# Kernel tuning notes

Hardware: AMD Instinct MI355X
Metric: run time of the kernel (lower is better)

The kernel has to match this reference:

```python
import jax, jax.numpy as jnp
import numpy as np
import math

B, H, S, D = 2, 8, 1024, 384
LAMBDA_INIT = 0.8 - 0.6 * math.exp(-0.3 * 1)  # depth = 1


def _clin(xr, xi, wr, wi, br=None, bi=None):
    # complex linear: (xr + i xi) @ (wr + i wi)^T + (br + i bi)
    o_r = jnp.einsum('bhse,de->bhsd', xr, wr) - jnp.einsum('bhse,de->bhsd', xi, wi)
    o_i = jnp.einsum('bhse,de->bhsd', xr, wi) + jnp.einsum('bhse,de->bhsd', xi, wr)
    if br is not None:
        o_r = o_r + br
        o_i = o_i + bi
    return o_r, o_i


def _attn_w(qr, qi, kr, ki, scale):
    # complex score magnitude -> softmax
    s_r = jnp.einsum('bhqd,bhkd->bhqk', qr, kr) + jnp.einsum('bhqd,bhkd->bhqk', qi, ki)
    s_i = jnp.einsum('bhqd,bhkd->bhqk', qi, kr) - jnp.einsum('bhqd,bhkd->bhqk', qr, ki)
    return jax.nn.softmax(jnp.sqrt(s_r ** 2 + s_i ** 2 + 1e-8) * scale, axis=-1)


def setup_inputs() -> dict:
    key = jax.random.key(0)
    ks = jax.random.split(key, 32)
    n = lambda k, sh, std=1.0: jax.random.normal(k, sh, dtype=jnp.float32) * std
    sd = 1.0 / math.sqrt(D)
    inp = {
        'q_r': n(ks[0], (B, H, S, D)), 'q_i': n(ks[1], (B, H, S, D)),
        'k_r': n(ks[2], (B, H, S, D)), 'k_i': n(ks[3], (B, H, S, D)),
        'v_r': n(ks[4], (B, H, S, D)), 'v_i': n(ks[5], (B, H, S, D)),
        'pe_q_r': n(ks[6], (B, H, S, D)), 'pe_q_i': n(ks[7], (B, H, S, D)),
        'pe_k_r': n(ks[8], (B, H, S, D)), 'pe_k_i': n(ks[9], (B, H, S, D)),
        'wq_r': n(ks[10], (2 * D, D), sd), 'wq_i': n(ks[11], (2 * D, D), sd),
        'bq_r': jnp.zeros((2 * D,), jnp.float32), 'bq_i': jnp.zeros((2 * D,), jnp.float32),
        'wk_r': n(ks[12], (D, D), sd), 'wk_i': n(ks[13], (D, D), sd),
        'bk_r': jnp.zeros((D,), jnp.float32), 'bk_i': jnp.zeros((D,), jnp.float32),
        'wv_r': n(ks[14], (D, D), sd), 'wv_i': n(ks[15], (D, D), sd),
        'bv_r': jnp.zeros((D,), jnp.float32), 'bv_i': jnp.zeros((D,), jnp.float32),
        'wg_r': n(ks[16], (D, D), sd), 'wg_i': n(ks[17], (D, D), sd),
        'bg_r': jnp.zeros((D,), jnp.float32), 'bg_i': jnp.zeros((D,), jnp.float32),
        'wo_r': n(ks[18], (D, D), sd), 'wo_i': n(ks[19], (D, D), sd),
        'bo_r': jnp.zeros((D,), jnp.float32), 'bo_i': jnp.zeros((D,), jnp.float32),
        'lam_q1': n(ks[20], (D,), 0.1), 'lam_k1': n(ks[21], (D,), 0.1),
        'lam_q2': n(ks[22], (D,), 0.1), 'lam_k2': n(ks[23], (D,), 0.1),
        'subln_w': jnp.ones((2 * D,), jnp.float32),
    }
    return inp


def reference(q_r, q_i, k_r, k_i, v_r, v_i, pe_q_r, pe_q_i, pe_k_r, pe_k_i,
              wq_r, wq_i, bq_r, bq_i, wk_r, wk_i, bk_r, bk_i,
              wv_r, wv_i, bv_r, bv_i, wg_r, wg_i, bg_r, bg_i,
              wo_r, wo_i, bo_r, bo_i, lam_q1, lam_k1, lam_q2, lam_k2, subln_w):
    scale = D ** (-0.5)
    qp_r, qp_i = _clin(q_r, q_i, wq_r, wq_i, bq_r, bq_i)   # [B,H,S,2D]
    kp_r, kp_i = _clin(k_r, k_i, wk_r, wk_i, bk_r, bk_i)   # [B,H,S,D]
    vp_r, vp_i = _clin(v_r, v_i, wv_r, wv_i, bv_r, bv_i)
    qp_r = qp_r + jnp.concatenate([pe_q_r, pe_q_r], axis=-1)
    qp_i = qp_i + jnp.concatenate([pe_q_i, pe_q_i], axis=-1)
    kp_r = kp_r + pe_k_r
    kp_i = kp_i + pe_k_i
    q1_r, q2_r = jnp.split(qp_r, 2, axis=-1)
    q1_i, q2_i = jnp.split(qp_i, 2, axis=-1)
    w1 = _attn_w(q1_r, q1_i, kp_r, kp_i, scale)
    w2 = _attn_w(q2_r, q2_i, kp_r, kp_i, scale)
    a1_r = jnp.einsum('bhqk,bhkd->bhqd', w1, vp_r)
    a1_i = jnp.einsum('bhqk,bhkd->bhqd', w1, vp_i)
    a2_r = jnp.einsum('bhqk,bhkd->bhqd', w2, vp_r)
    a2_i = jnp.einsum('bhqk,bhkd->bhqd', w2, vp_i)
    cat_r = jnp.concatenate([a1_r, a2_r], axis=-1)
    cat_i = jnp.concatenate([a1_i, a2_i], axis=-1)
    # complex RMSNorm (SubLN) over 2D dim
    rms = jnp.sqrt(jnp.mean(cat_r ** 2 + cat_i ** 2, axis=-1, keepdims=True) + 1e-5)
    cat_r = cat_r / rms * subln_w
    cat_i = cat_i / rms * subln_w
    a1_r, a2_r = jnp.split(cat_r, 2, axis=-1)
    a1_i, a2_i = jnp.split(cat_i, 2, axis=-1)
    lam1 = jnp.exp(jnp.sum(lam_q1 * lam_k1))
    lam2 = jnp.exp(jnp.sum(lam_q2 * lam_k2))
    lam = jax.nn.sigmoid(lam1 - lam2 + LAMBDA_INIT)
    out_r = a1_r - lam * a2_r
    out_i = a1_i - lam * a2_i
    g_r, g_i = _clin(q_r, q_i, wg_r, wg_i, bg_r, bg_i)
    out_r, out_i = g_r * out_r - g_i * out_i, g_r * out_i + g_i * out_r
    out_r, out_i = _clin(out_r, out_i, wo_r, wo_i, bo_r, bo_i)
    return (out_r, out_i)
```

## Files before the change

kernel.cpp:

```cpp
#include <hip/hip_runtime.h>
#include <cstdint>


typedef _Float16 f16;
typedef __attribute__((ext_vector_type(8))) _Float16 f16x8;
typedef __attribute__((ext_vector_type(4))) _Float16 f16x4;
typedef __attribute__((ext_vector_type(4))) float    f32x4;

#define NROW      16384L
#define HALF_OUT  6291456L
#define SCALE_QK  0.05103103630798288f
#define LAMBDA_INIT 0.35550906759096926f

__device__ __forceinline__ void gl2lds16(const void* g, void* l) {
  __builtin_amdgcn_global_load_lds(
      (const __attribute__((address_space(1))) void*)(uintptr_t)g,
      (__attribute__((address_space(3))) void*)(uint32_t)(uintptr_t)l,
      16, 0, 0);
}

enum { MODE_PROJ = 0, MODE_VT = 1, MODE_OUT = 2, MODE_PV = 3 };

template <int MODE>
__launch_bounds__(256, 2)
__global__ void gemm128(const f16* __restrict__ A, int lda,
                        const f16* __restrict__ W, int ldw,
                        const float* __restrict__ bias,
                        const f16* __restrict__ pe16, int pelim,
                        void* __restrict__ outp, void* __restrict__ outp2,
                        int ldo, int K, int gx)
{
  __shared__ f16 As[2][128 * 64];
  __shared__ f16 Bs[2][128 * 64];
  const int t    = threadIdx.x;
  const int lane = t & 63;
  const int wave = t >> 6;
  const int bid  = blockIdx.x;
  const int xcd  = bid & 7;
  const int per  = bid >> 3;

  long row0, col0;
  const f16 *Ab, *Wb;
  int bh = 0;
  if (MODE == MODE_PV) {
    bh = xcd * 2 + per / 96;
    const int rem = per % 96;
    row0 = (long)(rem / 6) * 128;
    col0 = (long)(rem % 6) * 128;
    const int slab = bh + (row0 >= 1024 ? 16 : 0);
    Ab = A + ((long)slab << 20) + (row0 & 1023) * (long)lda;
    Wb = W + (long)bh * 768 * 1024 + col0 * (long)ldw;
  } else {
    row0 = (long)(xcd * 16 + per / gx) * 128;
    col0 = (long)(per % gx) * 128;
    Ab = A + row0 * (long)lda;
    Wb = W + col0 * (long)ldw;
  }

  const int wm = (wave >> 1) * 64;
  const int wn = (wave & 1) * 64;
  const int lm = lane & 15;
  const int l4 = lane >> 4;

  f32x4 acc[4][4] = {};

  auto stage = [&](int kk, int sub) {
#pragma unroll
    for (int p = 0; p < 4; ++p) {
      int sg = p * 256 + t;
      int r = sg >> 3, cl = sg & 7, cg = cl ^ (r & 7);
      gl2lds16(Ab + (long)r * lda + kk + cg * 8, &As[sub][sg * 8]);
      gl2lds16(Wb + (long)r * ldw + kk + cg * 8, &Bs[sub][sg * 8]);
    }
  };

  const int NT = K >> 6;
  stage(0, 0);
  stage(64, 1);
  int cur = 0;
  for (int it = 0; it < NT; ++it) {
    if (it + 1 < NT) asm volatile("s_waitcnt vmcnt(8)" ::: "memory");
    else             asm volatile("s_waitcnt vmcnt(0)" ::: "memory");
    __builtin_amdgcn_s_barrier();
#pragma unroll
    for (int ks = 0; ks < 2; ++ks) {
      f16x8 bfr[4];
#pragma unroll
      for (int nt = 0; nt < 4; ++nt) {
        int rr = wn + nt * 16 + lm;
        bfr[nt] = *(const f16x8*)&Bs[cur][rr * 64 + (((ks * 4 + l4) ^ (rr & 7)) << 3)];
      }
#pragma unroll
      for (int mt = 0; mt < 4; ++mt) {
        int rr = wm + mt * 16 + lm;
        f16x8 afr = *(const f16x8*)&As[cur][rr * 64 + (((ks * 4 + l4) ^ (rr & 7)) << 3)];
#pragma unroll
        for (int nt = 0; nt < 4; ++nt)
          acc[mt][nt] = __builtin_amdgcn_mfma_f32_16x16x32_f16(afr, bfr[nt], acc[mt][nt], 0, 0, 0);
      }
    }
    __builtin_amdgcn_s_barrier();
    if (it + 2 < NT) stage((it + 2) << 6, cur);
    cur ^= 1;
  }

  const int lm4 = l4 * 4;
  const int ln  = lm;
#pragma unroll
  for (int mt = 0; mt < 4; ++mt) {
#pragma unroll
    for (int nt = 0; nt < 4; ++nt) {
      int col = (int)col0 + wn + nt * 16 + ln;
      if (MODE == MODE_VT) {
        long rowb = row0 + wm + mt * 16 + lm4;
        long vbh = rowb >> 10, sx = rowb & 1023;
        f16x4 v;
#pragma unroll
        for (int r = 0; r < 4; ++r) v[r] = (f16)(acc[mt][nt][r] + bias[col]);
        *(f16x4*)&((f16*)outp)[(vbh * 768 + col) * 1024 + sx] = v;
      } else if (MODE == MODE_PV) {
#pragma unroll
        for (int r = 0; r < 4; ++r) {
          long grow = row0 + wm + mt * 16 + lm4 + r;
          f16 val = (f16)acc[mt][nt][r];
          if (grow < 1024) ((f16*)outp )[((long)bh * 1024 + grow)        * 768 + col] = val;
          else             ((f16*)outp2)[((long)bh * 1024 + grow - 1024) * 768 + col] = val;
        }
      } else {
#pragma unroll
        for (int r = 0; r < 4; ++r) {
          long row = row0 + wm + mt * 16 + lm4 + r;
          float c = acc[mt][nt][r] + bias[col];
          if (MODE == MODE_PROJ) {
            if (col < pelim) {
              int pc = col < 768 ? col : col - 768;
              c += (float)pe16[row * 768 + pc];
            }
            ((f16*)outp)[row * (long)ldo + col] = (f16)c;
          } else {
            float* of = (float*)outp;
            if (col < 384) of[row * 384 + col] = c;
            else           of[HALF_OUT + row * 384 + (col - 384)] = c;
          }
        }
      }
    }
  }
}

__launch_bounds__(256, 2)
__global__ void score128(const f16* __restrict__ QG, const f16* __restrict__ Kc,
                         f16* __restrict__ P)
{
  __shared__ f16 AsL[2][128 * 32], AsH[2][128 * 32];
  __shared__ f16 BsL[2][128 * 32], BsH[2][128 * 32];
  const int t = threadIdx.x, lane = t & 63, wave = t >> 6;
  const int bid = blockIdx.x;
  const int xcd = bid & 7, per = bid >> 3;
  const int z   = xcd * 4 + per / 64;
  const int rem = per % 64;
  const int w = z >> 4, bh = z & 15;
  const long row0 = (long)(rem / 8) * 128, col0 = (long)(rem % 8) * 128;
  const f16* A = QG + (long)bh * 1024 * 2304 + row0 * 2304 + w * 768;
  const f16* B = Kc + (long)bh * 1024 * 768 + col0 * 768;
  f16* Pz = P + ((long)z << 20);

  const int wm = (wave >> 1) * 64, wn = (wave & 1) * 64;
  const int lm = lane & 15, l4 = lane >> 4;
  f32x4 accr[4][4] = {}, acci[4][4] = {};

  auto stage = [&](int kk, int sub) {
#pragma unroll
    for (int p = 0; p < 2; ++p) {
      int sg = p * 256 + t;
      int r = sg >> 2, cl = sg & 3, cg = cl ^ (r & 3);
      gl2lds16(A + (long)r * 2304 + kk + cg * 8,       &AsL[sub][sg * 8]);
      gl2lds16(A + (long)r * 2304 + 384 + kk + cg * 8, &AsH[sub][sg * 8]);
      gl2lds16(B + (long)r * 768 + kk + cg * 8,        &BsL[sub][sg * 8]);
      gl2lds16(B + (long)r * 768 + 384 + kk + cg * 8,  &BsH[sub][sg * 8]);
    }
  };

  stage(0, 0);
  stage(32, 1);
  int cur = 0;
  for (int it = 0; it < 12; ++it) {
    if (it + 1 < 12) asm volatile("s_waitcnt vmcnt(8)" ::: "memory");
    else             asm volatile("s_waitcnt vmcnt(0)" ::: "memory");
    __builtin_amdgcn_s_barrier();
    f16x8 bl[4], bh2[4];
#pragma unroll
    for (int nt = 0; nt < 4; ++nt) {
      int rr = wn + nt * 16 + lm;
      int off = rr * 32 + (((l4 ^ (rr & 3))) << 3);
      bl[nt]  = *(const f16x8*)&BsL[cur][off];
      bh2[nt] = *(const f16x8*)&BsH[cur][off];
    }
#pragma unroll
    for (int mt = 0; mt < 4; ++mt) {
      int rr = wm + mt * 16 + lm;
      int off = rr * 32 + (((l4 ^ (rr & 3))) << 3);
      f16x8 al  = *(const f16x8*)&AsL[cur][off];
      f16x8 ah  = *(const f16x8*)&AsH[cur][off];
      f16x8 nal = -al;
#pragma unroll
      for (int nt = 0; nt < 4; ++nt) {
        accr[mt][nt] = __builtin_amdgcn_mfma_f32_16x16x32_f16(al,  bl[nt],  accr[mt][nt], 0, 0, 0);
        accr[mt][nt] = __builtin_amdgcn_mfma_f32_16x16x32_f16(ah,  bh2[nt], accr[mt][nt], 0, 0, 0);
        acci[mt][nt] = __builtin_amdgcn_mfma_f32_16x16x32_f16(ah,  bl[nt],  acci[mt][nt], 0, 0, 0);
        acci[mt][nt] = __builtin_amdgcn_mfma_f32_16x16x32_f16(nal, bh2[nt], acci[mt][nt], 0, 0, 0);
      }
    }
    __builtin_amdgcn_s_barrier();
    if (it + 2 < 12) stage((it + 2) << 5, cur);
    cur ^= 1;
  }
  const int lm4 = l4 * 4, ln = lm;
#pragma unroll
  for (int mt = 0; mt < 4; ++mt)
#pragma unroll
    for (int nt = 0; nt < 4; ++nt) {
      int col = (int)col0 + wn + nt * 16 + ln;
#pragma unroll
      for (int r = 0; r < 4; ++r) {
        long row = row0 + wm + mt * 16 + lm4 + r;
        float sr = accr[mt][nt][r], si = acci[mt][nt][r];
        float m = sqrtf(sr * sr + si * si + 1e-8f) * SCALE_QK;
        Pz[row * 1024 + col] = (f16)m;
      }
    }
}

__global__ void softmax_kernel(f16* __restrict__ P)
{
  const long row = (long)blockIdx.x * 4 + (threadIdx.x >> 6);
  f16* p = P + row * 1024;
  const int lane = threadIdx.x & 63;
  f16x8 v0 = *(const f16x8*)(p + lane * 16);
  f16x8 v1 = *(const f16x8*)(p + lane * 16 + 8);
  float x[16];
#pragma unroll
  for (int i = 0; i < 8; ++i) { x[i] = (float)v0[i]; x[8 + i] = (float)v1[i]; }
  float m = x[0];
#pragma unroll
  for (int i = 1; i < 16; ++i) m = fmaxf(m, x[i]);
#pragma unroll
  for (int off = 1; off < 64; off <<= 1) m = fmaxf(m, __shfl_xor(m, off));
  float s = 0.f;
#pragma unroll
  for (int i = 0; i < 16; ++i) { x[i] = __expf(x[i] - m); s += x[i]; }
#pragma unroll
  for (int off = 1; off < 64; off <<= 1) s += __shfl_xor(s, off);
  float inv = 1.f / s;
  f16x8 o0, o1;
#pragma unroll
  for (int i = 0; i < 8; ++i) { o0[i] = (f16)(x[i] * inv); o1[i] = (f16)(x[8 + i] * inv); }
  *(f16x8*)(p + lane * 16)     = o0;
  *(f16x8*)(p + lane * 16 + 8) = o1;
}

__global__ void fuse_kernel(const f16* __restrict__ A1, const f16* __restrict__ A2,
                            const f16* __restrict__ QG, const float* __restrict__ subw,
                            const float* __restrict__ lamp, f16* __restrict__ Xatt)
{
  const long row = blockIdx.x;
  const int t = threadIdx.x, lane = t & 63, wv = t >> 6;
  const f16* a1 = A1 + row * 768;
  const f16* a2 = A2 + row * 768;
  const f16* g  = QG + row * 2304 + 1536;
  float a1r[3], a1i[3], a2r[3], a2i[3];
  float ss = 0.f;
#pragma unroll
  for (int q = 0; q < 3; ++q) {
    int d = t + q * 128;
    a1r[q] = (float)a1[d]; a1i[q] = (float)a1[d + 384];
    a2r[q] = (float)a2[d]; a2i[q] = (float)a2[d + 384];
    ss += a1r[q] * a1r[q] + a1i[q] * a1i[q] + a2r[q] * a2r[q] + a2i[q] * a2i[q];
  }
#pragma unroll
  for (int m = 1; m < 64; m <<= 1) ss += __shfl_xor(ss, m);
  __shared__ float part[2];
  if (lane == 0) part[wv] = ss;
  __syncthreads();
  float inv = rsqrtf((part[0] + part[1]) * (1.f / 768.f) + 1e-5f);
  float lam = lamp[0];
#pragma unroll
  for (int q = 0; q < 3; ++q) {
    int d = t + q * 128;
    float w1 = subw[d], w2 = subw[d + 384];
    float n1r = a1r[q] * inv * w1, n1i = a1i[q] * inv * w1;
    float n2r = a2r[q] * inv * w2, n2i = a2i[q] * inv * w2;
    float orr = n1r - lam * n2r, oii = n1i - lam * n2i;
    float gr = (float)g[d], gi = (float)g[d + 384];
    Xatt[row * 768 + d]       = (f16)(gr * orr - gi * oii);
    Xatt[row * 768 + d + 384] = (f16)(gr * oii + gi * orr);
  }
}

__global__ void lam_kernel(const float* lq1, const float* lk1,
                           const float* lq2, const float* lk2, float* out)
{
  const int t = threadIdx.x, lane = t & 63, wv = t >> 6;
  float s1 = 0.f, s2 = 0.f;
#pragma unroll
  for (int q = 0; q < 3; ++q) {
    int d = t + q * 128;
    s1 += lq1[d] * lk1[d];
    s2 += lq2[d] * lk2[d];
  }
#pragma unroll
  for (int m = 1; m < 64; m <<= 1) { s1 += __shfl_xor(s1, m); s2 += __shfl_xor(s2, m); }
  __shared__ float p1[2], p2[2];
  if (lane == 0) { p1[wv] = s1; p2[wv] = s2; }
  __syncthreads();
  if (t == 0) {
    float x = expf(p1[0] + p1[1]) - expf(p2[0] + p2[1]) + LAMBDA_INIT;
    out[0] = 1.f / (1.f + expf(-x));
  }
}

__global__ void pack_x(const float* __restrict__ xr, const float* __restrict__ xi,
                       f16* __restrict__ X)
{
  long i = (long)blockIdx.x * 256 + threadIdx.x;
  long row = i / 96;
  int  rem = (int)(i - row * 96);
  int  c   = rem * 8;
  const float* src = (c < 384) ? (xr + row * 384 + c) : (xi + row * 384 + (c - 384));
  f16x8 o;
#pragma unroll
  for (int j = 0; j < 8; ++j) o[j] = (f16)src[j];
  *(f16x8*)&X[row * 768 + c] = o;
}

__global__ void pack_wq(const float* wq_r, const float* wq_i,
                        const float* wg_r, const float* wg_i,
                        const float* bq_r, const float* bq_i,
                        const float* bg_r, const float* bg_i,
                        f16* __restrict__ Wp, float* __restrict__ bp)
{
  long i = (long)blockIdx.x * 256 + threadIdx.x;
  int n = (int)(i / 768), e = (int)(i % 768);
  int s = n / 384, d = n - s * 384;
  int hb = (e >= 384);
  int ee = e - hb * 384;
  float v = 0.f, b = 0.f;
  switch (s) {
    case 0: v = hb ? -wq_i[d * 384 + ee]         :  wq_r[d * 384 + ee];         b = bq_r[d];       break;
    case 1: v = hb ?  wq_r[d * 384 + ee]         :  wq_i[d * 384 + ee];         b = bq_i[d];       break;
    case 2: v = hb ? -wq_i[(384 + d) * 384 + ee] :  wq_r[(384 + d) * 384 + ee]; b = bq_r[384 + d]; break;
    case 3: v = hb ?  wq_r[(384 + d) * 384 + ee] :  wq_i[(384 + d) * 384 + ee]; b = bq_i[384 + d]; break;
    case 4: v = hb ? -wg_i[d * 384 + ee]         :  wg_r[d * 384 + ee];         b = bg_r[d];       break;
    case 5: v = hb ?  wg_r[d * 384 + ee]         :  wg_i[d * 384 + ee];         b = bg_i[d];       break;
  }
  Wp[i] = (f16)v;
  if (e == 0) bp[n] = b;
}

__global__ void pack_w_std(const float* wr, const float* wi,
                           const float* br, const float* bi,
                           f16* __restrict__ Wp, float* __restrict__ bp)
{
  long i = (long)blockIdx.x * 256 + threadIdx.x;
  int n = (int)(i / 768), e = (int)(i % 768);
  int hb = (e >= 384);
  int ee = e - hb * 384;
  float v, b;
  if (n < 384) { v = hb ? -wi[n * 384 + ee] : wr[n * 384 + ee]; b = br[n]; }
  else { int d = n - 384; v = hb ? wr[d * 384 + ee] : wi[d * 384 + ee]; b = bi[d]; }
  Wp[i] = (f16)v;
  if (e == 0) bp[n] = b;
}

extern "C" void kernel_launch(void* const* d_in, const int* in_sizes, int n_in,
                              void* d_out, int out_size, void* d_ws, size_t ws_size,
                              hipStream_t stream)
{
  const float* q_r    = (const float*)d_in[0];
  const float* q_i    = (const float*)d_in[1];
  const float* k_r    = (const float*)d_in[2];
  const float* k_i    = (const float*)d_in[3];
  const float* v_r    = (const float*)d_in[4];
  const float* v_i    = (const float*)d_in[5];
  const float* pe_q_r = (const float*)d_in[6];
  const float* pe_q_i = (const float*)d_in[7];
  const float* pe_k_r = (const float*)d_in[8];
  const float* pe_k_i = (const float*)d_in[9];
  const float* wq_r = (const float*)d_in[10];
  const float* wq_i = (const float*)d_in[11];
  const float* bq_r = (const float*)d_in[12];
  const float* bq_i = (const float*)d_in[13];
  const float* wk_r = (const float*)d_in[14];
  const float* wk_i = (const float*)d_in[15];
  const float* bk_r = (const float*)d_in[16];
  const float* bk_i = (const float*)d_in[17];
  const float* wv_r = (const float*)d_in[18];
  const float* wv_i = (const float*)d_in[19];
  const float* bv_r = (const float*)d_in[20];
  const float* bv_i = (const float*)d_in[21];
  const float* wg_r = (const float*)d_in[22];
  const float* wg_i = (const float*)d_in[23];
  const float* bg_r = (const float*)d_in[24];
  const float* bg_i = (const float*)d_in[25];
  const float* wo_r = (const float*)d_in[26];
  const float* wo_i = (const float*)d_in[27];
  const float* bo_r = (const float*)d_in[28];
  const float* bo_i = (const float*)d_in[29];
  const float* lam_q1 = (const float*)d_in[30];
  const float* lam_k1 = (const float*)d_in[31];
  const float* lam_q2 = (const float*)d_in[32];
  const float* lam_k2 = (const float*)d_in[33];
  const float* subln_w = (const float*)d_in[34];

  char* base = (char*)d_ws;
  size_t off = 0;
  auto alloc = [&](size_t bytes) -> void* {
    void* p = base + off;
    off = (off + bytes + 255) & ~(size_t)255;
    return p;
  };
  f16*   Wq   = (f16*)alloc(2304L * 768 * 2);
  f16*   Wk   = (f16*)alloc(768L * 768 * 2);
  f16*   Wv   = (f16*)alloc(768L * 768 * 2);
  f16*   Wo   = (f16*)alloc(768L * 768 * 2);
  float* bq   = (float*)alloc(2304 * 4);
  float* bk   = (float*)alloc(768 * 4);
  float* bv   = (float*)alloc(768 * 4);
  float* bo   = (float*)alloc(768 * 4);
  float* lamp = (float*)alloc(4);
  f16*   X    = (f16*)alloc(NROW * 768 * 2);
  f16*   QG   = (f16*)alloc(NROW * 2304 * 2);
  f16*   Kc   = (f16*)alloc(NROW * 768 * 2);
  f16*   Vt   = (f16*)alloc(16L * 768 * 1024 * 2);
  f16*   P    = (f16*)alloc(32L * 1024 * 1024 * 2);
  if (off > ws_size) return;
  f16* A1   = Kc;
  f16* A2   = X;
  f16* Xatt = Vt;
  f16* PEQ  = P;
  f16* PEK  = P + NROW * 768;

  pack_wq<<<6912, 256, 0, stream>>>(wq_r, wq_i, wg_r, wg_i, bq_r, bq_i, bg_r, bg_i, Wq, bq);
  pack_w_std<<<2304, 256, 0, stream>>>(wk_r, wk_i, bk_r, bk_i, Wk, bk);
  pack_w_std<<<2304, 256, 0, stream>>>(wv_r, wv_i, bv_r, bv_i, Wv, bv);
  pack_w_std<<<2304, 256, 0, stream>>>(wo_r, wo_i, bo_r, bo_i, Wo, bo);
  lam_kernel<<<1, 128, 0, stream>>>(lam_q1, lam_k1, lam_q2, lam_k2, lamp);
  pack_x<<<6144, 256, 0, stream>>>(pe_q_r, pe_q_i, PEQ);
  pack_x<<<6144, 256, 0, stream>>>(pe_k_r, pe_k_i, PEK);

  pack_x<<<6144, 256, 0, stream>>>(q_r, q_i, X);
  gemm128<MODE_PROJ><<<2304, 256, 0, stream>>>(
      X, 768, Wq, 768, bq, PEQ, 1536, QG, nullptr, 2304, 768, 18);

  pack_x<<<6144, 256, 0, stream>>>(k_r, k_i, X);
  gemm128<MODE_PROJ><<<768, 256, 0, stream>>>(
      X, 768, Wk, 768, bk, PEK, 768, Kc, nullptr, 768, 768, 6);

  pack_x<<<6144, 256, 0, stream>>>(v_r, v_i, X);
  gemm128<MODE_VT><<<768, 256, 0, stream>>>(
      X, 768, Wv, 768, bv, nullptr, 0, Vt, nullptr, 0, 768, 6);

  score128<<<2048, 256, 0, stream>>>(QG, Kc, P);
  softmax_kernel<<<8192, 256, 0, stream>>>(P);
  gemm128<MODE_PV><<<1536, 256, 0, stream>>>(
      P, 1024, Vt, 1024, nullptr, nullptr, 0, A1, A2, 0, 1024, 0);

  fuse_kernel<<<16384, 128, 0, stream>>>(A1, A2, QG, subln_w, lamp, Xatt);

  gemm128<MODE_OUT><<<768, 256, 0, stream>>>(
      Xatt, 768, Wo, 768, bo, nullptr, 0, d_out, nullptr, 0, 768, 6);

  (void)in_sizes; (void)n_in; (void)out_size;
}
```

Baseline: 763.4 us.

## Merge prep kernels and fuse Q/K/V projections into one launch

Folds all weight packing, input packing and the lambda reduction into a single prep kernel, then runs the Q, K and V projections as one grouped GEMM launch. The fp16 packed K and V inputs are staged in the output buffer so all three can coexist. The score kernel's LDS layout also changes from four 32-wide split buffers to two 64-wide swizzled buffers. The aim is to cut launch count and the tail idle time between small GEMMs, at the cost of more branching per block and reuse of the output buffer as scratch.

```diff
diff --git a/kernel.cpp b/kernel.cpp
--- a/kernel.cpp
+++ b/kernel.cpp
@@ -111,14 +111,7 @@
 #pragma unroll
     for (int nt = 0; nt < 4; ++nt) {
       int col = (int)col0 + wn + nt * 16 + ln;
-      if (MODE == MODE_VT) {
-        long rowb = row0 + wm + mt * 16 + lm4;
-        long vbh = rowb >> 10, sx = rowb & 1023;
-        f16x4 v;
-#pragma unroll
-        for (int r = 0; r < 4; ++r) v[r] = (f16)(acc[mt][nt][r] + bias[col]);
-        *(f16x4*)&((f16*)outp)[(vbh * 768 + col) * 1024 + sx] = v;
-      } else if (MODE == MODE_PV) {
+      if (MODE == MODE_PV) {
 #pragma unroll
         for (int r = 0; r < 4; ++r) {
           long grow = row0 + wm + mt * 16 + lm4 + r;
@@ -131,17 +124,109 @@
         for (int r = 0; r < 4; ++r) {
           long row = row0 + wm + mt * 16 + lm4 + r;
           float c = acc[mt][nt][r] + bias[col];
-          if (MODE == MODE_PROJ) {
-            if (col < pelim) {
-              int pc = col < 768 ? col : col - 768;
-              c += (float)pe16[row * 768 + pc];
-            }
-            ((f16*)outp)[row * (long)ldo + col] = (f16)c;
-          } else {
-            float* of = (float*)outp;
-            if (col < 384) of[row * 384 + col] = c;
-            else           of[HALF_OUT + row * 384 + (col - 384)] = c;
+          float* of = (float*)outp;
+          if (col < 384) of[row * 384 + col] = c;
+          else           of[HALF_OUT + row * 384 + (col - 384)] = c;
+        }
+      }
+    }
+  }
+}
+
+__launch_bounds__(256, 2)
+__global__ void proj_all(const f16* __restrict__ Xq, const f16* __restrict__ Xk,
+                         const f16* __restrict__ Xv,
+                         const f16* __restrict__ Wq, const f16* __restrict__ Wk,
+                         const f16* __restrict__ Wv,
+                         const float* __restrict__ bq, const float* __restrict__ bk,
+                         const float* __restrict__ bv,
+                         const f16* __restrict__ PEQ, const f16* __restrict__ PEK,
+                         f16* __restrict__ QG, f16* __restrict__ Kc,
+                         f16* __restrict__ Vt)
+{
+  __shared__ f16 As[2][128 * 64];
+  __shared__ f16 Bs[2][128 * 64];
+  const int t = threadIdx.x, lane = t & 63, wave = t >> 6;
+  const int bid = blockIdx.x;
+
+  const f16 *A, *W; const float* bias; const f16* pe;
+  int pelim, gx, ldo, lb; f16* outp; bool vt = false;
+  if (bid < 2304)      { A = Xq; W = Wq; bias = bq; pe = PEQ; pelim = 1536; gx = 18; outp = QG; ldo = 2304; lb = bid; }
+  else if (bid < 3072) { A = Xk; W = Wk; bias = bk; pe = PEK; pelim = 768;  gx = 6;  outp = Kc; ldo = 768;  lb = bid - 2304; }
+  else                 { A = Xv; W = Wv; bias = bv; pe = nullptr; pelim = 0; gx = 6; outp = Vt; ldo = 0;    lb = bid - 3072; vt = true; }
+
+  const int xcd = lb & 7, per = lb >> 3;
+  const long row0 = (long)(xcd * 16 + per / gx) * 128;
+  const long col0 = (long)(per % gx) * 128;
+  const f16* Ab = A + row0 * 768;
+  const f16* Wb = W + col0 * 768;
+
+  const int wm = (wave >> 1) * 64, wn = (wave & 1) * 64;
+  const int lm = lane & 15, l4 = lane >> 4;
+  f32x4 acc[4][4] = {};
+
+  auto stage = [&](int kk, int sub) {
+#pragma unroll
+    for (int p = 0; p < 4; ++p) {
+      int sg = p * 256 + t;
+      int r = sg >> 3, cl = sg & 7, cg = cl ^ (r & 7);
+      gl2lds16(Ab + (long)r * 768 + kk + cg * 8, &As[sub][sg * 8]);
+      gl2lds16(Wb + (long)r * 768 + kk + cg * 8, &Bs[sub][sg * 8]);
+    }
+  };
+
+  stage(0, 0);
+  stage(64, 1);
+  int cur = 0;
+  for (int it = 0; it < 12; ++it) {
+    if (it + 1 < 12) asm volatile("s_waitcnt vmcnt(8)" ::: "memory");
+    else             asm volatile("s_waitcnt vmcnt(0)" ::: "memory");
+    __builtin_amdgcn_s_barrier();
+#pragma unroll
+    for (int ks = 0; ks < 2; ++ks) {
+      f16x8 bfr[4];
+#pragma unroll
+      for (int nt = 0; nt < 4; ++nt) {
+        int rr = wn + nt * 16 + lm;
+        bfr[nt] = *(const f16x8*)&Bs[cur][rr * 64 + (((ks * 4 + l4) ^ (rr & 7)) << 3)];
+      }
+#pragma unroll
+      for (int mt = 0; mt < 4; ++mt) {
+        int rr = wm + mt * 16 + lm;
+        f16x8 afr = *(const f16x8*)&As[cur][rr * 64 + (((ks * 4 + l4) ^ (rr & 7)) << 3)];
+#pragma unroll
+        for (int nt = 0; nt < 4; ++nt)
+          acc[mt][nt] = __builtin_amdgcn_mfma_f32_16x16x32_f16(afr, bfr[nt], acc[mt][nt], 0, 0, 0);
+      }
+    }
+    __builtin_amdgcn_s_barrier();
+    if (it + 2 < 12) stage((it + 2) << 6, cur);
+    cur ^= 1;
+  }
+
+  const int lm4 = l4 * 4, ln = lm;
+#pragma unroll
+  for (int mt = 0; mt < 4; ++mt) {
+#pragma unroll
+    for (int nt = 0; nt < 4; ++nt) {
+      int col = (int)col0 + wn + nt * 16 + ln;
+      if (vt) {
+        long rowb = row0 + wm + mt * 16 + lm4;
+        long vbh = rowb >> 10, sx = rowb & 1023;
+        f16x4 v;
+#pragma unroll
+        for (int r = 0; r < 4; ++r) v[r] = (f16)(acc[mt][nt][r] + bias[col]);
+        *(f16x4*)&Vt[(vbh * 768 + col) * 1024 + sx] = v;
+      } else {
+#pragma unroll
+        for (int r = 0; r < 4; ++r) {
+          long row = row0 + wm + mt * 16 + lm4 + r;
+          float c = acc[mt][nt][r] + bias[col];
+          if (col < pelim) {
+            int pc = col < 768 ? col : col - 768;
+            c += (float)pe[row * 768 + pc];
           }
+          outp[row * (long)ldo + col] = (f16)c;
         }
       }
     }
@@ -152,8 +237,8 @@
 __global__ void score128(const f16* __restrict__ QG, const f16* __restrict__ Kc,
                          f16* __restrict__ P)
 {
-  __shared__ f16 AsL[2][128 * 32], AsH[2][128 * 32];
-  __shared__ f16 BsL[2][128 * 32], BsH[2][128 * 32];
+  __shared__ f16 As[2][128 * 64];
+  __shared__ f16 Bs[2][128 * 64];
   const int t = threadIdx.x, lane = t & 63, wave = t >> 6;
   const int bid = blockIdx.x;
   const int xcd = bid & 7, per = bid >> 3;
@@ -171,13 +256,15 @@
 
   auto stage = [&](int kk, int sub) {
 #pragma unroll
-    for (int p = 0; p < 2; ++p) {
+    for (int p = 0; p < 4; ++p) {
       int sg = p * 256 + t;
-      int r = sg >> 2, cl = sg & 3, cg = cl ^ (r & 3);
-      gl2lds16(A + (long)r * 2304 + kk + cg * 8,       &AsL[sub][sg * 8]);
-      gl2lds16(A + (long)r * 2304 + 384 + kk + cg * 8, &AsH[sub][sg * 8]);
-      gl2lds16(B + (long)r * 768 + kk + cg * 8,        &BsL[sub][sg * 8]);
-      gl2lds16(B + (long)r * 768 + 384 + kk + cg * 8,  &BsH[sub][sg * 8]);
+      int r = sg >> 3, c = sg & 7, cg = c ^ (r & 7);
+      const f16* sa = (cg < 4) ? A + (long)r * 2304 + kk + cg * 8
+                               : A + (long)r * 2304 + 384 + kk + (cg - 4) * 8;
+      gl2lds16(sa, &As[sub][sg * 8]);
+      const f16* sb = (cg < 4) ? B + (long)r * 768 + kk + cg * 8
+                               : B + (long)r * 768 + 384 + kk + (cg - 4) * 8;
+      gl2lds16(sb, &Bs[sub][sg * 8]);
     }
   };
 
@@ -192,16 +279,14 @@
 #pragma unroll
     for (int nt = 0; nt < 4; ++nt) {
       int rr = wn + nt * 16 + lm;
-      int off = rr * 32 + (((l4 ^ (rr & 3))) << 3);
-      bl[nt]  = *(const f16x8*)&BsL[cur][off];
-      bh2[nt] = *(const f16x8*)&BsH[cur][off];
+      bl[nt]  = *(const f16x8*)&Bs[cur][rr * 64 + ((l4 ^ (rr & 7)) << 3)];
+      bh2[nt] = *(const f16x8*)&Bs[cur][rr * 64 + (((l4 + 4) ^ (rr & 7)) << 3)];
     }
 #pragma unroll
     for (int mt = 0; mt < 4; ++mt) {
       int rr = wm + mt * 16 + lm;
-      int off = rr * 32 + (((l4 ^ (rr & 3))) << 3);
-      f16x8 al  = *(const f16x8*)&AsL[cur][off];
-      f16x8 ah  = *(const f16x8*)&AsH[cur][off];
+      f16x8 al  = *(const f16x8*)&As[cur][rr * 64 + ((l4 ^ (rr & 7)) << 3)];
+      f16x8 ah  = *(const f16x8*)&As[cur][rr * 64 + (((l4 + 4) ^ (rr & 7)) << 3)];
       f16x8 nal = -al;
 #pragma unroll
       for (int nt = 0; nt < 4; ++nt) {
@@ -297,119 +382,100 @@
   }
 }
 
-__global__ void lam_kernel(const float* lq1, const float* lk1,
-                           const float* lq2, const float* lk2, float* out)
-{
-  const int t = threadIdx.x, lane = t & 63, wv = t >> 6;
-  float s1 = 0.f, s2 = 0.f;
-#pragma unroll
-  for (int q = 0; q < 3; ++q) {
-    int d = t + q * 128;
-    s1 += lq1[d] * lk1[d];
-    s2 += lq2[d] * lk2[d];
-  }
-#pragma unroll
-  for (int m = 1; m < 64; m <<= 1) { s1 += __shfl_xor(s1, m); s2 += __shfl_xor(s2, m); }
-  __shared__ float p1[2], p2[2];
-  if (lane == 0) { p1[wv] = s1; p2[wv] = s2; }
-  __syncthreads();
-  if (t == 0) {
-    float x = expf(p1[0] + p1[1]) - expf(p2[0] + p2[1]) + LAMBDA_INIT;
-    out[0] = 1.f / (1.f + expf(-x));
-  }
-}
-
-__global__ void pack_x(const float* __restrict__ xr, const float* __restrict__ xi,
-                       f16* __restrict__ X)
-{
-  long i = (long)blockIdx.x * 256 + threadIdx.x;
-  long row = i / 96;
-  int  rem = (int)(i - row * 96);
-  int  c   = rem * 8;
-  const float* src = (c < 384) ? (xr + row * 384 + c) : (xi + row * 384 + (c - 384));
-  f16x8 o;
-#pragma unroll
-  for (int j = 0; j < 8; ++j) o[j] = (f16)src[j];
-  *(f16x8*)&X[row * 768 + c] = o;
-}
-
-__global__ void pack_wq(const float* wq_r, const float* wq_i,
-                        const float* wg_r, const float* wg_i,
-                        const float* bq_r, const float* bq_i,
-                        const float* bg_r, const float* bg_i,
-                        f16* __restrict__ Wp, float* __restrict__ bp)
-{
-  long i = (long)blockIdx.x * 256 + threadIdx.x;
-  int n = (int)(i / 768), e = (int)(i % 768);
-  int s = n / 384, d = n - s * 384;
-  int hb = (e >= 384);
-  int ee = e - hb * 384;
-  float v = 0.f, b = 0.f;
-  switch (s) {
-    case 0: v = hb ? -wq_i[d * 384 + ee]         :  wq_r[d * 384 + ee];         b = bq_r[d];       break;
-    case 1: v = hb ?  wq_r[d * 384 + ee]         :  wq_i[d * 384 + ee];         b = bq_i[d];       break;
-    case 2: v = hb ? -wq_i[(384 + d) * 384 + ee] :  wq_r[(384 + d) * 384 + ee]; b = bq_r[384 + d]; break;
-    case 3: v = hb ?  wq_r[(384 + d) * 384 + ee] :  wq_i[(384 + d) * 384 + ee]; b = bq_i[384 + d]; break;
-    case 4: v = hb ? -wg_i[d * 384 + ee]         :  wg_r[d * 384 + ee];         b = bg_r[d];       break;
-    case 5: v = hb ?  wg_r[d * 384 + ee]         :  wg_i[d * 384 + ee];         b = bg_i[d];       break;
-  }
-  Wp[i] = (f16)v;
-  if (e == 0) bp[n] = b;
-}
-
-__global__ void pack_w_std(const float* wr, const float* wi,
-                           const float* br, const float* bi,
-                           f16* __restrict__ Wp, float* __restrict__ bp)
-{
-  long i = (long)blockIdx.x * 256 + threadIdx.x;
-  int n = (int)(i / 768), e = (int)(i % 768);
-  int hb = (e >= 384);
-  int ee = e - hb * 384;
-  float v, b;
-  if (n < 384) { v = hb ? -wi[n * 384 + ee] : wr[n * 384 + ee]; b = br[n]; }
-  else { int d = n - 384; v = hb ? wr[d * 384 + ee] : wi[d * 384 + ee]; b = bi[d]; }
-  Wp[i] = (f16)v;
-  if (e == 0) bp[n] = b;
+struct PrepArgs {
+  const float *wq_r, *wq_i, *wg_r, *wg_i, *bq_r, *bq_i, *bg_r, *bg_i;
+  const float *wk_r, *wk_i, *bk_r, *bk_i;
+  const float *wv_r, *wv_i, *bv_r, *bv_i;
+  const float *wo_r, *wo_i, *bo_r, *bo_i;
+  const float *q_r, *q_i, *k_r, *k_i, *v_r, *v_i;
+  const float *pe_q_r, *pe_q_i, *pe_k_r, *pe_k_i;
+  const float *lq1, *lk1, *lq2, *lk2;
+  f16 *Wq, *Wk, *Wv, *Wo;
+  float *bq, *bk, *bv, *bo, *lamp;
+  f16 *Xq, *Xk, *Xv, *PEQ, *PEK;
+};
+
+__global__ void prep_kernel(PrepArgs a)
+{
+  const int bid = blockIdx.x, t = threadIdx.x;
+  __shared__ float p1[4], p2[4];
+  if (bid < 6912) {
+    long i = (long)bid * 256 + t;
+    int n = (int)(i / 768), e = (int)(i % 768);
+    int s = n / 384, d = n - s * 384;
+    int hb = (e >= 384);
+    int ee = e - hb * 384;
+    float v = 0.f, b = 0.f;
+    switch (s) {
+      case 0: v = hb ? -a.wq_i[d * 384 + ee]         :  a.wq_r[d * 384 + ee];         b = a.bq_r[d];       break;
+      case 1: v = hb ?  a.wq_r[d * 384 + ee]         :  a.wq_i[d * 384 + ee];         b = a.bq_i[d];       break;
+      case 2: v = hb ? -a.wq_i[(384 + d) * 384 + ee] :  a.wq_r[(384 + d) * 384 + ee]; b = a.bq_r[384 + d]; break;
+      case 3: v = hb ?  a.wq_r[(384 + d) * 384 + ee] :  a.wq_i[(384 + d) * 384 + ee]; b = a.bq_i[384 + d]; break;
+      case 4: v = hb ? -a.wg_i[d * 384 + ee]         :  a.wg_r[d * 384 + ee];         b = a.bg_r[d];       break;
+      case 5: v = hb ?  a.wg_r[d * 384 + ee]         :  a.wg_i[d * 384 + ee];         b = a.bg_i[d];       break;
+    }
+    a.Wq[i] = (f16)v;
+    if (e == 0) a.bq[n] = b;
+  } else if (bid < 13824) {
+    int sel = (bid - 6912) / 2304, lb = (bid - 6912) % 2304;
+    const float *wr, *wi, *br, *bi; f16* Wp; float* bp;
+    if (sel == 0)      { wr = a.wk_r; wi = a.wk_i; br = a.bk_r; bi = a.bk_i; Wp = a.Wk; bp = a.bk; }
+    else if (sel == 1) { wr = a.wv_r; wi = a.wv_i; br = a.bv_r; bi = a.bv_i; Wp = a.Wv; bp = a.bv; }
+    else               { wr = a.wo_r; wi = a.wo_i; br = a.bo_r; bi = a.bo_i; Wp = a.Wo; bp = a.bo; }
+    long i = (long)lb * 256 + t;
+    int n = (int)(i / 768), e = (int)(i % 768);
+    int hb = (e >= 384);
+    int ee = e - hb * 384;
+    float v, b;
+    if (n < 384) { v = hb ? -wi[n * 384 + ee] : wr[n * 384 + ee]; b = br[n]; }
+    else { int d = n - 384; v = hb ? wr[d * 384 + ee] : wi[d * 384 + ee]; b = bi[d]; }
+    Wp[i] = (f16)v;
+    if (e == 0) bp[n] = b;
+  } else if (bid < 44544) {
+    int sel = (bid - 13824) / 6144, lb = (bid - 13824) % 6144;
+    const float *xr, *xi; f16* X;
+    switch (sel) {
+      case 0: xr = a.q_r;    xi = a.q_i;    X = a.Xq;  break;
+      case 1: xr = a.k_r;    xi = a.k_i;    X = a.Xk;  break;
+      case 2: xr = a.v_r;    xi = a.v_i;    X = a.Xv;  break;
+      case 3: xr = a.pe_q_r; xi = a.pe_q_i; X = a.PEQ; break;
+      default: xr = a.pe_k_r; xi = a.pe_k_i; X = a.PEK; break;
+    }
+    long i = (long)lb * 256 + t;
+    long row = i / 96;
+    int  rem = (int)(i - row * 96);
+    int  c   = rem * 8;
+    const float* src = (c < 384) ? (xr + row * 384 + c) : (xi + row * 384 + (c - 384));
+    f16x8 o;
+#pragma unroll
+    for (int j = 0; j < 8; ++j) o[j] = (f16)src[j];
+    *(f16x8*)&X[row * 768 + c] = o;
+  } else {
+    const int lane = t & 63, wv = t >> 6;
+    float s1 = 0.f, s2 = 0.f;
+    if (t < 128) {
+#pragma unroll
+      for (int q = 0; q < 3; ++q) {
+        int d = t + q * 128;
+        s1 += a.lq1[d] * a.lk1[d];
+        s2 += a.lq2[d] * a.lk2[d];
+      }
+    }
+#pragma unroll
+    for (int m = 1; m < 64; m <<= 1) { s1 += __shfl_xor(s1, m); s2 += __shfl_xor(s2, m); }
+    if (lane == 0) { p1[wv] = s1; p2[wv] = s2; }
+    __syncthreads();
+    if (t == 0) {
+      float x = expf(p1[0] + p1[1] + p1[2] + p1[3]) - expf(p2[0] + p2[1] + p2[2] + p2[3]) + LAMBDA_INIT;
+      a.lamp[0] = 1.f / (1.f + expf(-x));
+    }
+  }
 }
 
 extern "C" void kernel_launch(void* const* d_in, const int* in_sizes, int n_in,
                               void* d_out, int out_size, void* d_ws, size_t ws_size,
                               hipStream_t stream)
 {
-  const float* q_r    = (const float*)d_in[0];
-  const float* q_i    = (const float*)d_in[1];
-  const float* k_r    = (const float*)d_in[2];
-  const float* k_i    = (const float*)d_in[3];
-  const float* v_r    = (const float*)d_in[4];
-  const float* v_i    = (const float*)d_in[5];
-  const float* pe_q_r = (const float*)d_in[6];
-  const float* pe_q_i = (const float*)d_in[7];
-  const float* pe_k_r = (const float*)d_in[8];
-  const float* pe_k_i = (const float*)d_in[9];
-  const float* wq_r = (const float*)d_in[10];
-  const float* wq_i = (const float*)d_in[11];
-  const float* bq_r = (const float*)d_in[12];
-  const float* bq_i = (const float*)d_in[13];
-  const float* wk_r = (const float*)d_in[14];
-  const float* wk_i = (const float*)d_in[15];
-  const float* bk_r = (const float*)d_in[16];
-  const float* bk_i = (const float*)d_in[17];
-  const float* wv_r = (const float*)d_in[18];
-  const float* wv_i = (const float*)d_in[19];
-  const float* bv_r = (const float*)d_in[20];
-  const float* bv_i = (const float*)d_in[21];
-  const float* wg_r = (const float*)d_in[22];
-  const float* wg_i = (const float*)d_in[23];
-  const float* bg_r = (const float*)d_in[24];
-  const float* bg_i = (const float*)d_in[25];
-  const float* wo_r = (const float*)d_in[26];
-  const float* wo_i = (const float*)d_in[27];
-  const float* bo_r = (const float*)d_in[28];
-  const float* bo_i = (const float*)d_in[29];
-  const float* lam_q1 = (const float*)d_in[30];
-  const float* lam_k1 = (const float*)d_in[31];
-  const float* lam_q2 = (const float*)d_in[32];
-  const float* lam_k2 = (const float*)d_in[33];
   const float* subln_w = (const float*)d_in[34];
 
   char* base = (char*)d_ws;
@@ -439,26 +505,35 @@
   f16* Xatt = Vt;
   f16* PEQ  = P;
   f16* PEK  = P + NROW * 768;
-
-  pack_wq<<<6912, 256, 0, stream>>>(wq_r, wq_i, wg_r, wg_i, bq_r, bq_i, bg_r, bg_i, Wq, bq);
-  pack_w_std<<<2304, 256, 0, stream>>>(wk_r, wk_i, bk_r, bk_i, Wk, bk);
-  pack_w_std<<<2304, 256, 0, stream>>>(wv_r, wv_i, bv_r, bv_i, Wv, bv);
-  pack_w_std<<<2304, 256, 0, stream>>>(wo_r, wo_i, bo_r, bo_i, Wo, bo);
-  lam_kernel<<<1, 128, 0, stream>>>(lam_q1, lam_k1, lam_q2, lam_k2, lamp);
-  pack_x<<<6144, 256, 0, stream>>>(pe_q_r, pe_q_i, PEQ);
-  pack_x<<<6144, 256, 0, stream>>>(pe_k_r, pe_k_i, PEK);
-
-  pack_x<<<6144, 256, 0, stream>>>(q_r, q_i, X);
-  gemm128<MODE_PROJ><<<2304, 256, 0, stream>>>(
-      X, 768, Wq, 768, bq, PEQ, 1536, QG, nullptr, 2304, 768, 18);
-
-  pack_x<<<6144, 256, 0, stream>>>(k_r, k_i, X);
-  gemm128<MODE_PROJ><<<768, 256, 0, stream>>>(
-      X, 768, Wk, 768, bk, PEK, 768, Kc, nullptr, 768, 768, 6);
-
-  pack_x<<<6144, 256, 0, stream>>>(v_r, v_i, X);
-  gemm128<MODE_VT><<<768, 256, 0, stream>>>(
-      X, 768, Wv, 768, bv, nullptr, 0, Vt, nullptr, 0, 768, 6);
+  f16* Xk   = (f16*)d_out;
+  f16* Xv   = Xk + NROW * 768;
+
+  PrepArgs pa;
+  pa.wq_r = (const float*)d_in[10]; pa.wq_i = (const float*)d_in[11];
+  pa.wg_r = (const float*)d_in[22]; pa.wg_i = (const float*)d_in[23];
+  pa.bq_r = (const float*)d_in[12]; pa.bq_i = (const float*)d_in[13];
+  pa.bg_r = (const float*)d_in[24]; pa.bg_i = (const float*)d_in[25];
+  pa.wk_r = (const float*)d_in[14]; pa.wk_i = (const float*)d_in[15];
+  pa.bk_r = (const float*)d_in[16]; pa.bk_i = (const float*)d_in[17];
+  pa.wv_r = (const float*)d_in[18]; pa.wv_i = (const float*)d_in[19];
+  pa.bv_r = (const float*)d_in[20]; pa.bv_i = (const float*)d_in[21];
+  pa.wo_r = (const float*)d_in[26]; pa.wo_i = (const float*)d_in[27];
+  pa.bo_r = (const float*)d_in[28]; pa.bo_i = (const float*)d_in[29];
+  pa.q_r = (const float*)d_in[0]; pa.q_i = (const float*)d_in[1];
+  pa.k_r = (const float*)d_in[2]; pa.k_i = (const float*)d_in[3];
+  pa.v_r = (const float*)d_in[4]; pa.v_i = (const float*)d_in[5];
+  pa.pe_q_r = (const float*)d_in[6]; pa.pe_q_i = (const float*)d_in[7];
+  pa.pe_k_r = (const float*)d_in[8]; pa.pe_k_i = (const float*)d_in[9];
+  pa.lq1 = (const float*)d_in[30]; pa.lk1 = (const float*)d_in[31];
+  pa.lq2 = (const float*)d_in[32]; pa.lk2 = (const float*)d_in[33];
+  pa.Wq = Wq; pa.Wk = Wk; pa.Wv = Wv; pa.Wo = Wo;
+  pa.bq = bq; pa.bk = bk; pa.bv = bv; pa.bo = bo; pa.lamp = lamp;
+  pa.Xq = X; pa.Xk = Xk; pa.Xv = Xv; pa.PEQ = PEQ; pa.PEK = PEK;
+
+  prep_kernel<<<44545, 256, 0, stream>>>(pa);
+
+  proj_all<<<3840, 256, 0, stream>>>(X, Xk, Xv, Wq, Wk, Wv, bq, bk, bv,
+                                     PEQ, PEK, QG, Kc, Vt);
 
   score128<<<2048, 256, 0, stream>>>(QG, Kc, P);
   softmax_kernel<<<8192, 256, 0, stream>>>(P);
```

New measurement: 748.2 us. 2.0% less time.
